# Performance work log

Measured on AMD Instinct MI355X. Metric: run time of the kernel, lower is better.

## Reference

```python
import jax, jax.numpy as jnp
import numpy as np


def setup_inputs() -> dict:
    key = jax.random.key(0)
    ks = jax.random.split(key, 6)
    B, N, d = 8, 2048, 64
    h = jax.random.normal(ks[0], (B, N, d), dtype=jnp.float32)
    adj = jax.random.randint(ks[1], (B, N, N), 0, 2, dtype=jnp.int32)
    h_root = jax.random.normal(ks[2], (B, N), dtype=jnp.float32)
    weight = jax.random.normal(ks[3], (d, d), dtype=jnp.float32) * (1.0 / np.sqrt(d))
    a1 = jax.random.normal(ks[4], (d, 1), dtype=jnp.float32) * (1.0 / np.sqrt(d))
    a2 = jax.random.normal(ks[5], (d, 1), dtype=jnp.float32) * (1.0 / np.sqrt(d))
    return {"h": h, "adj": adj, "h_root": h_root, "weight": weight, "a1": a1, "a2": a2}


def reference(h, adj, h_root, weight, a1, a2):
    h0 = h
    hw = jax.nn.relu(jnp.matmul(h, weight))          # (B,N,d)
    t1 = jnp.matmul(hw, a1)                          # (B,N,1)
    t2 = jnp.matmul(hw, a2)                          # (B,N,1)
    # e[b,i,j] = relu(t1[b,i] + t2[b,j])  (broadcast, same as repeat/view in torch)
    e = jax.nn.relu(t1 + jnp.swapaxes(t2, -1, -2))   # (B,N,N)
    # FAITHFUL to source bug: pos0 = -9e15 * zeros_like(adj) == 0, so
    # non-edges get logit 0 (not -inf) before softmax.
    e = jnp.where(adj > 0, e, jnp.zeros_like(e))
    attention = jax.nn.softmax(e, axis=-1)           # (B,N,N)
    embedding = jnp.matmul(attention, hw)            # (B,N,d)
    # assign = h_root[:,:,None] @ ones(B,1,d) -> h_root broadcast over d;
    # assign > 0  <=>  h_root > 0 since ones are positive.
    assign = h_root[:, :, None] * jnp.ones((1, 1, hw.shape[-1]), dtype=hw.dtype)
    embedding = jnp.where(assign > 0, embedding, h0)
    return embedding
```

## Files before the change

### kernel.cpp

```cpp
#include <hip/hip_runtime.h>
#include <hip/hip_bf16.h>

#define BATCH 8
#define NN    2048
#define DD    64
#define BN    (BATCH * NN)

typedef __attribute__((ext_vector_type(8))) short bf16x8;
typedef __attribute__((ext_vector_type(4))) float f32x4;

static __device__ __forceinline__ unsigned f2bf_pk(float lo, float hi) {
  unsigned ul = __float_as_uint(lo);
  unsigned uh = __float_as_uint(hi);
  ul = (ul + 0x7fffu + ((ul >> 16) & 1u)) >> 16;
  uh = (uh + 0x7fffu + ((uh >> 16) & 1u)) & 0xffff0000u;
  return ul | uh;
}

__global__ __launch_bounds__(256) void k1_hw_t1_t2(
    const float* __restrict__ h, const float* __restrict__ W,
    const float* __restrict__ a1, const float* __restrict__ a2,
    unsigned short* __restrict__ hwT, float* __restrict__ t1, float* __restrict__ t2) {
  __shared__ float ht[64 * 36];
  __shared__ float Ws[64 * 64];
  __shared__ unsigned short bt[64 * 40];

  const int t  = threadIdx.x;
  const int r0 = blockIdx.x * 32;

#pragma unroll
  for (int r = 0; r < 4; ++r) {
    int f = t + 256 * r;
    reinterpret_cast<float4*>(Ws)[f] = reinterpret_cast<const float4*>(W)[f];
  }
#pragma unroll
  for (int r = 0; r < 2; ++r) {
    int f = t + 256 * r;
    int i = f >> 4, j4 = f & 15;
    float4 v = reinterpret_cast<const float4*>(h + (size_t)(r0 + i) * DD)[j4];
    ht[(4 * j4 + 0) * 36 + i] = v.x;
    ht[(4 * j4 + 1) * 36 + i] = v.y;
    ht[(4 * j4 + 2) * 36 + i] = v.z;
    ht[(4 * j4 + 3) * 36 + i] = v.w;
  }
  __syncthreads();

  const int trow = t >> 4, kcol = t & 15;
  float4 acc0 = make_float4(0.f, 0.f, 0.f, 0.f);
  float4 acc1 = make_float4(0.f, 0.f, 0.f, 0.f);

#pragma unroll 8
  for (int j = 0; j < 64; ++j) {
    float2 hv = *reinterpret_cast<const float2*>(&ht[j * 36 + 2 * trow]);
    float4 wv = reinterpret_cast<const float4*>(Ws)[j * 16 + kcol];
    acc0.x = fmaf(hv.x, wv.x, acc0.x); acc0.y = fmaf(hv.x, wv.y, acc0.y);
    acc0.z = fmaf(hv.x, wv.z, acc0.z); acc0.w = fmaf(hv.x, wv.w, acc0.w);
    acc1.x = fmaf(hv.y, wv.x, acc1.x); acc1.y = fmaf(hv.y, wv.y, acc1.y);
    acc1.z = fmaf(hv.y, wv.z, acc1.z); acc1.w = fmaf(hv.y, wv.w, acc1.w);
  }

  acc0.x = fmaxf(acc0.x, 0.f); acc0.y = fmaxf(acc0.y, 0.f);
  acc0.z = fmaxf(acc0.z, 0.f); acc0.w = fmaxf(acc0.w, 0.f);
  acc1.x = fmaxf(acc1.x, 0.f); acc1.y = fmaxf(acc1.y, 0.f);
  acc1.z = fmaxf(acc1.z, 0.f); acc1.w = fmaxf(acc1.w, 0.f);

  float4 a1v = reinterpret_cast<const float4*>(a1)[kcol];
  float4 a2v = reinterpret_cast<const float4*>(a2)[kcol];
  float s1_0 = acc0.x * a1v.x + acc0.y * a1v.y + acc0.z * a1v.z + acc0.w * a1v.w;
  float s1_1 = acc1.x * a1v.x + acc1.y * a1v.y + acc1.z * a1v.z + acc1.w * a1v.w;
  float s2_0 = acc0.x * a2v.x + acc0.y * a2v.y + acc0.z * a2v.z + acc0.w * a2v.w;
  float s2_1 = acc1.x * a2v.x + acc1.y * a2v.y + acc1.z * a2v.z + acc1.w * a2v.w;
#pragma unroll
  for (int m = 1; m <= 8; m <<= 1) {
    s1_0 += __shfl_xor(s1_0, m, 64);
    s1_1 += __shfl_xor(s1_1, m, 64);
    s2_0 += __shfl_xor(s2_0, m, 64);
    s2_1 += __shfl_xor(s2_1, m, 64);
  }
  {
    int row = r0 + 2 * trow;
    if (kcol == 0) {
      t1[row] = s1_0; t1[row + 1] = s1_1;
      t2[row] = s2_0; t2[row + 1] = s2_1;
    }
  }

  {
    const float* a0 = &acc0.x;
    const float* a1p = &acc1.x;
#pragma unroll
    for (int c = 0; c < 4; ++c) {
      int k = 4 * kcol + c;
      *reinterpret_cast<unsigned*>(&bt[k * 40 + 2 * trow]) = f2bf_pk(a0[c], a1p[c]);
    }
  }
  __syncthreads();
  {
    int k = t >> 2, jp = t & 3;
    int bb = r0 >> 11;
    int jb = r0 & (NN - 1);
    *reinterpret_cast<int4*>(hwT + ((size_t)bb * DD + k) * NN + jb + jp * 8) =
        *reinterpret_cast<const int4*>(&bt[k * 40 + jp * 8]);
  }
}

#define JCHUNK 128
#define LDST   136

__global__ __launch_bounds__(256, 2) void k2_attn(
    const unsigned short* __restrict__ hwT, const int* __restrict__ adj,
    const float* __restrict__ t1, const float* __restrict__ t2,
    float* __restrict__ pacc, float* __restrict__ pden, int nsplit) {
  __shared__ unsigned short hws[2][64 * LDST];
  __shared__ float t2s[2][JCHUNK];

  const int t     = threadIdx.x;
  const int split = blockIdx.x >> 8;
  const int rem   = blockIdx.x & 255;
  const int b     = rem >> 5;
  const int i0    = (rem & 31) * 64;
  const int w     = t >> 6;
  const int lane  = t & 63;
  const int m     = lane & 15;
  const int quad  = lane >> 4;

  const int jspan  = NN / nsplit;
  const int jbase  = split * jspan;
  const int chunks = jspan / JCHUNK;

  const float t1v = t1[b * NN + i0 + w * 16 + m];
  const int*  adjl = adj + (size_t)(b * NN + i0 + w * 16 + m) * NN + jbase + quad * 8;
  const unsigned short* hwTb = hwT + (size_t)b * DD * NN;
  const float* t2b = t2 + b * NN + jbase;

  f32x4 acc[4];
#pragma unroll
  for (int g = 0; g < 4; ++g) acc[g] = (f32x4){0.f, 0.f, 0.f, 0.f};
  float den = 0.f;

  int4   sreg[4];
  float4 t2reg;
  int4   adjv[8], adjn[8];

  auto stage_load = [&](int c) {
    const unsigned short* src = hwTb + jbase + c * JCHUNK;
#pragma unroll
    for (int r = 0; r < 4; ++r) {
      int idx = t + 256 * r, k = idx >> 4, jp = idx & 15;
      sreg[r] = *reinterpret_cast<const int4*>(src + (size_t)k * NN + jp * 8);
    }
    if (t < 32) t2reg = *reinterpret_cast<const float4*>(t2b + c * JCHUNK + t * 4);
  };
  auto stage_write = [&](int buf) {
#pragma unroll
    for (int r = 0; r < 4; ++r) {
      int idx = t + 256 * r, k = idx >> 4, jp = idx & 15;
      *reinterpret_cast<int4*>(&hws[buf][k * LDST + jp * 8]) = sreg[r];
    }
    if (t < 32) *reinterpret_cast<float4*>(&t2s[buf][t * 4]) = t2reg;
  };
  auto load_adj = [&](int c, int4* dst) {
    const int* ap = adjl + c * JCHUNK;
#pragma unroll
    for (int ks = 0; ks < 4; ++ks) {
      dst[2 * ks]     = *reinterpret_cast<const int4*>(ap + ks * 32);
      dst[2 * ks + 1] = *reinterpret_cast<const int4*>(ap + ks * 32 + 4);
    }
  };

  load_adj(0, adjv);
  stage_load(0);
  stage_write(0);
  __syncthreads();

  int buf = 0;
  for (int c = 0; c < chunks; ++c) {
    if (c + 1 < chunks) { stage_load(c + 1); load_adj(c + 1, adjn); }

#pragma unroll
    for (int ks = 0; ks < 4; ++ks) {
      float4 e0 = *reinterpret_cast<const float4*>(&t2s[buf][ks * 32 + quad * 8]);
      float4 e1 = *reinterpret_cast<const float4*>(&t2s[buf][ks * 32 + quad * 8 + 4]);
      int4 A0 = adjv[2 * ks], A1 = adjv[2 * ks + 1];
      float p0 = (A0.x > 0) ? __expf(fmaxf(t1v + e0.x, 0.f)) : 1.f;
      float p1 = (A0.y > 0) ? __expf(fmaxf(t1v + e0.y, 0.f)) : 1.f;
      float p2 = (A0.z > 0) ? __expf(fmaxf(t1v + e0.z, 0.f)) : 1.f;
      float p3 = (A0.w > 0) ? __expf(fmaxf(t1v + e0.w, 0.f)) : 1.f;
      float p4 = (A1.x > 0) ? __expf(fmaxf(t1v + e1.x, 0.f)) : 1.f;
      float p5 = (A1.y > 0) ? __expf(fmaxf(t1v + e1.y, 0.f)) : 1.f;
      float p6 = (A1.z > 0) ? __expf(fmaxf(t1v + e1.z, 0.f)) : 1.f;
      float p7 = (A1.w > 0) ? __expf(fmaxf(t1v + e1.w, 0.f)) : 1.f;
      den += ((p0 + p1) + (p2 + p3)) + ((p4 + p5) + (p6 + p7));

      union { bf16x8 v; unsigned u[4]; } Af;
      Af.u[0] = f2bf_pk(p0, p1);
      Af.u[1] = f2bf_pk(p2, p3);
      Af.u[2] = f2bf_pk(p4, p5);
      Af.u[3] = f2bf_pk(p6, p7);

#pragma unroll
      for (int g = 0; g < 4; ++g) {
        bf16x8 Bf = *reinterpret_cast<const bf16x8*>(
            &hws[buf][(g * 16 + m) * LDST + ks * 32 + quad * 8]);
        acc[g] = __builtin_amdgcn_mfma_f32_16x16x32_bf16(Af.v, Bf, acc[g], 0, 0, 0);
      }
    }

    if (c + 1 < chunks) {
      stage_write(buf ^ 1);
#pragma unroll
      for (int r = 0; r < 8; ++r) adjv[r] = adjn[r];
    }
    __syncthreads();
    buf ^= 1;
  }

  den += __shfl_xor(den, 16, 64);
  den += __shfl_xor(den, 32, 64);

  const size_t obase = (size_t)split * BN + (size_t)b * NN + i0 + w * 16;
  if (quad == 0) pden[obase + m] = den;
#pragma unroll
  for (int g = 0; g < 4; ++g)
#pragma unroll
    for (int r = 0; r < 4; ++r)
      pacc[(obase + quad * 4 + r) * DD + g * 16 + m] = acc[g][r];
}

__global__ __launch_bounds__(256) void k3_reduce(
    const float* __restrict__ pacc, const float* __restrict__ pden,
    const float* __restrict__ h, const float* __restrict__ h_root,
    float* __restrict__ out, int nsplit) {
  const int g   = blockIdx.x * 256 + threadIdx.x;
  const int row = g >> 4;
  const int k4  = g & 15;

  float4 a = make_float4(0.f, 0.f, 0.f, 0.f);
  float den = 0.f;
  for (int s = 0; s < nsplit; ++s) {
    const size_t prow = (size_t)s * BN + row;
    float4 p = reinterpret_cast<const float4*>(pacc + prow * DD)[k4];
    a.x += p.x; a.y += p.y; a.z += p.z; a.w += p.w;
    den += pden[prow];
  }
  const float hr = h_root[row];
  float4 res;
  if (hr > 0.f) {
    const float inv = 1.f / den;
    res.x = a.x * inv; res.y = a.y * inv; res.z = a.z * inv; res.w = a.w * inv;
  } else {
    res = reinterpret_cast<const float4*>(h)[g];
  }
  reinterpret_cast<float4*>(out)[g] = res;
}

extern "C" void kernel_launch(void* const* d_in, const int* in_sizes, int n_in,
                              void* d_out, int out_size, void* d_ws, size_t ws_size,
                              hipStream_t stream) {
  const float* h      = (const float*)d_in[0];
  const int*   adj    = (const int*)d_in[1];
  const float* h_root = (const float*)d_in[2];
  const float* W      = (const float*)d_in[3];
  const float* a1     = (const float*)d_in[4];
  const float* a2     = (const float*)d_in[5];
  float* out = (float*)d_out;

  unsigned short* hwT = (unsigned short*)d_ws;
  float* t1 = (float*)(hwT + (size_t)BN * DD);
  float* t2 = t1 + BN;
  float* pacc = t2 + BN;

  int nsplit = 2;
  {
    size_t need = (size_t)BN * DD * 2 + sizeof(float) * (2 * (size_t)BN +
                  (size_t)nsplit * ((size_t)BN * DD + BN));
    if (need > ws_size) nsplit = 1;
  }
  float* pden = pacc + (size_t)nsplit * BN * DD;

  k1_hw_t1_t2<<<BN / 32, 256, 0, stream>>>(h, W, a1, a2, hwT, t1, t2);
  k2_attn<<<nsplit * 256, 256, 0, stream>>>(hwT, adj, t1, t2, pacc, pden, nsplit);
  k3_reduce<<<(BN * DD / 4) / 256, 256, 0, stream>>>(pacc, pden, h, h_root, out,
                                                     nsplit);
}
```

Measured before the change: 222.5 us.

## Split j range four ways, preload whole hw slice to LDS, coalesce partial stores

Raises the split of the attention kernel's j dimension from 2 to 4 (1024 blocks). Each block now loads its entire 512-column bf16 hw slice and t2 slice into shared memory once, which removes the per-chunk double buffering and barriers. Partial accumulators are staged through LDS so they can be written to global memory as coalesced float4 stores. In exchange, the partial-sum buffers and the reduce pass grow, LDS per block rises (about 67 KB), and the workspace-size fallback check is gone.

```diff
diff --git a/kernel.cpp b/kernel.cpp
--- a/kernel.cpp
+++ b/kernel.cpp
@@ -5,6 +5,12 @@
 #define NN    2048
 #define DD    64
 #define BN    (BATCH * NN)
+
+#define NSPLIT 4
+#define JSPAN  (NN / NSPLIT)
+#define JCHUNK 128
+#define CHUNKS (JSPAN / JCHUNK)
+#define HWST   520
 
 typedef __attribute__((ext_vector_type(8))) short bf16x8;
 typedef __attribute__((ext_vector_type(4))) float f32x4;
@@ -104,15 +110,12 @@
   }
 }
 
-#define JCHUNK 128
-#define LDST   136
-
 __global__ __launch_bounds__(256, 2) void k2_attn(
     const unsigned short* __restrict__ hwT, const int* __restrict__ adj,
     const float* __restrict__ t1, const float* __restrict__ t2,
-    float* __restrict__ pacc, float* __restrict__ pden, int nsplit) {
-  __shared__ unsigned short hws[2][64 * LDST];
-  __shared__ float t2s[2][JCHUNK];
+    float* __restrict__ pacc, float* __restrict__ pden) {
+  __shared__ unsigned short hws[64 * HWST];
+  __shared__ float t2s[JSPAN];
 
   const int t     = threadIdx.x;
   const int split = blockIdx.x >> 8;
@@ -123,42 +126,28 @@
   const int lane  = t & 63;
   const int m     = lane & 15;
   const int quad  = lane >> 4;
-
-  const int jspan  = NN / nsplit;
-  const int jbase  = split * jspan;
-  const int chunks = jspan / JCHUNK;
+  const int jbase = split * JSPAN;
+
+  const unsigned short* hwTb = hwT + (size_t)b * DD * NN + jbase;
+#pragma unroll
+  for (int r = 0; r < 16; ++r) {
+    int idx = t + 256 * r, k = idx >> 6, jp = idx & 63;
+    *reinterpret_cast<int4*>(&hws[k * HWST + jp * 8]) =
+        *reinterpret_cast<const int4*>(hwTb + (size_t)k * NN + jp * 8);
+  }
+  if (t < JSPAN / 4)
+    *reinterpret_cast<float4*>(&t2s[t * 4]) =
+        *reinterpret_cast<const float4*>(t2 + b * NN + jbase + t * 4);
 
   const float t1v = t1[b * NN + i0 + w * 16 + m];
-  const int*  adjl = adj + (size_t)(b * NN + i0 + w * 16 + m) * NN + jbase + quad * 8;
-  const unsigned short* hwTb = hwT + (size_t)b * DD * NN;
-  const float* t2b = t2 + b * NN + jbase;
+  const int* adjl = adj + (size_t)(b * NN + i0 + w * 16 + m) * NN + jbase + quad * 8;
 
   f32x4 acc[4];
 #pragma unroll
   for (int g = 0; g < 4; ++g) acc[g] = (f32x4){0.f, 0.f, 0.f, 0.f};
   float den = 0.f;
 
-  int4   sreg[4];
-  float4 t2reg;
-  int4   adjv[8], adjn[8];
-
-  auto stage_load = [&](int c) {
-    const unsigned short* src = hwTb + jbase + c * JCHUNK;
-#pragma unroll
-    for (int r = 0; r < 4; ++r) {
-      int idx = t + 256 * r, k = idx >> 4, jp = idx & 15;
-      sreg[r] = *reinterpret_cast<const int4*>(src + (size_t)k * NN + jp * 8);
-    }
-    if (t < 32) t2reg = *reinterpret_cast<const float4*>(t2b + c * JCHUNK + t * 4);
-  };
-  auto stage_write = [&](int buf) {
-#pragma unroll
-    for (int r = 0; r < 4; ++r) {
-      int idx = t + 256 * r, k = idx >> 4, jp = idx & 15;
-      *reinterpret_cast<int4*>(&hws[buf][k * LDST + jp * 8]) = sreg[r];
-    }
-    if (t < 32) *reinterpret_cast<float4*>(&t2s[buf][t * 4]) = t2reg;
-  };
+  int4 adjv[8], adjn[8];
   auto load_adj = [&](int c, int4* dst) {
     const int* ap = adjl + c * JCHUNK;
 #pragma unroll
@@ -169,18 +158,17 @@
   };
 
   load_adj(0, adjv);
-  stage_load(0);
-  stage_write(0);
-  __syncthreads();
-
-  int buf = 0;
-  for (int c = 0; c < chunks; ++c) {
-    if (c + 1 < chunks) { stage_load(c + 1); load_adj(c + 1, adjn); }
+  __syncthreads();
+
+#pragma unroll
+  for (int c = 0; c < CHUNKS; ++c) {
+    if (c + 1 < CHUNKS) load_adj(c + 1, adjn);
 
 #pragma unroll
     for (int ks = 0; ks < 4; ++ks) {
-      float4 e0 = *reinterpret_cast<const float4*>(&t2s[buf][ks * 32 + quad * 8]);
-      float4 e1 = *reinterpret_cast<const float4*>(&t2s[buf][ks * 32 + quad * 8 + 4]);
+      const float* t2p = &t2s[c * JCHUNK + ks * 32 + quad * 8];
+      float4 e0 = *reinterpret_cast<const float4*>(t2p);
+      float4 e1 = *reinterpret_cast<const float4*>(t2p + 4);
       int4 A0 = adjv[2 * ks], A1 = adjv[2 * ks + 1];
       float p0 = (A0.x > 0) ? __expf(fmaxf(t1v + e0.x, 0.f)) : 1.f;
       float p1 = (A0.y > 0) ? __expf(fmaxf(t1v + e0.y, 0.f)) : 1.f;
@@ -201,43 +189,51 @@
 #pragma unroll
       for (int g = 0; g < 4; ++g) {
         bf16x8 Bf = *reinterpret_cast<const bf16x8*>(
-            &hws[buf][(g * 16 + m) * LDST + ks * 32 + quad * 8]);
+            &hws[(g * 16 + m) * HWST + c * JCHUNK + ks * 32 + quad * 8]);
         acc[g] = __builtin_amdgcn_mfma_f32_16x16x32_bf16(Af.v, Bf, acc[g], 0, 0, 0);
       }
     }
 
-    if (c + 1 < chunks) {
-      stage_write(buf ^ 1);
+    if (c + 1 < CHUNKS) {
 #pragma unroll
       for (int r = 0; r < 8; ++r) adjv[r] = adjn[r];
     }
-    __syncthreads();
-    buf ^= 1;
   }
 
   den += __shfl_xor(den, 16, 64);
   den += __shfl_xor(den, 32, 64);
 
-  const size_t obase = (size_t)split * BN + (size_t)b * NN + i0 + w * 16;
-  if (quad == 0) pden[obase + m] = den;
+  const size_t sbase = (size_t)split * BN + (size_t)b * NN + i0;
+  if (quad == 0) pden[sbase + w * 16 + m] = den;
+
+  __syncthreads();
+  float* os = reinterpret_cast<float*>(hws);
 #pragma unroll
   for (int g = 0; g < 4; ++g)
 #pragma unroll
     for (int r = 0; r < 4; ++r)
-      pacc[(obase + quad * 4 + r) * DD + g * 16 + m] = acc[g][r];
+      os[(w * 16 + quad * 4 + r) * 68 + g * 16 + m] = acc[g][r];
+  __syncthreads();
+#pragma unroll
+  for (int r2 = 0; r2 < 4; ++r2) {
+    int idx = t + 256 * r2, row = idx >> 4, c4 = idx & 15;
+    *reinterpret_cast<float4*>(&pacc[(sbase + row) * DD + c4 * 4]) =
+        *reinterpret_cast<const float4*>(&os[row * 68 + c4 * 4]);
+  }
 }
 
 __global__ __launch_bounds__(256) void k3_reduce(
     const float* __restrict__ pacc, const float* __restrict__ pden,
     const float* __restrict__ h, const float* __restrict__ h_root,
-    float* __restrict__ out, int nsplit) {
+    float* __restrict__ out) {
   const int g   = blockIdx.x * 256 + threadIdx.x;
   const int row = g >> 4;
   const int k4  = g & 15;
 
   float4 a = make_float4(0.f, 0.f, 0.f, 0.f);
   float den = 0.f;
-  for (int s = 0; s < nsplit; ++s) {
+#pragma unroll
+  for (int s = 0; s < NSPLIT; ++s) {
     const size_t prow = (size_t)s * BN + row;
     float4 p = reinterpret_cast<const float4*>(pacc + prow * DD)[k4];
     a.x += p.x; a.y += p.y; a.z += p.z; a.w += p.w;
@@ -269,17 +265,9 @@
   float* t1 = (float*)(hwT + (size_t)BN * DD);
   float* t2 = t1 + BN;
   float* pacc = t2 + BN;
-
-  int nsplit = 2;
-  {
-    size_t need = (size_t)BN * DD * 2 + sizeof(float) * (2 * (size_t)BN +
-                  (size_t)nsplit * ((size_t)BN * DD + BN));
-    if (need > ws_size) nsplit = 1;
-  }
-  float* pden = pacc + (size_t)nsplit * BN * DD;
+  float* pden = pacc + (size_t)NSPLIT * BN * DD;
 
   k1_hw_t1_t2<<<BN / 32, 256, 0, stream>>>(h, W, a1, a2, hwT, t1, t2);
-  k2_attn<<<nsplit * 256, 256, 0, stream>>>(hwT, adj, t1, t2, pacc, pden, nsplit);
-  k3_reduce<<<(BN * DD / 4) / 256, 256, 0, stream>>>(pacc, pden, h, h_root, out,
-                                                     nsplit);
-}
+  k2_attn<<<NSPLIT * 256, 256, 0, stream>>>(hwT, adj, t1, t2, pacc, pden);
+  k3_reduce<<<(BN * DD / 4) / 256, 256, 0, stream>>>(pacc, pden, h, h_root, out);
+}
```

Measured after the change: 216.1 us. -2.9%, faster.
